# Kernel tuning notes

Measured on AMD Instinct MI355X. Metric: run time of the kernel, lower is better.

The kernel has to match this reference:

```python
import jax, jax.numpy as jnp
import numpy as np
from jax import lax

P_COARSE, P_FINE = 8, 4
EMBED_DIM = 128


def _patchify(x, p):
    # torch unfold(kernel=p, stride=p) then transpose: [B, Hp*Wp, C*p*p]
    B, C, H, W = x.shape
    Hp, Wp = H // p, W // p
    t = x.reshape(B, C, Hp, p, Wp, p).transpose(0, 2, 4, 1, 3, 5)
    return t.reshape(B, Hp * Wp, C * p * p), Hp, Wp


def _edge_map(x):
    gray = x.mean(axis=1, keepdims=True)
    kx = jnp.array([[-1., 0., 1.], [-2., 0., 2.], [-1., 0., 1.]], gray.dtype)[None, None]
    ky = jnp.array([[-1., -2., -1.], [0., 0., 0.], [1., 2., 1.]], gray.dtype)[None, None]
    pad = [(1, 1), (1, 1)]
    sx = lax.conv_general_dilated(gray, kx, (1, 1), pad)
    sy = lax.conv_general_dilated(gray, ky, (1, 1), pad)
    e = jnp.sqrt(sx * sx + sy * sy)
    B, _, H, W = e.shape
    # avg_pool2d(4, stride=4)
    return e.reshape(B, 1, H // 4, 4, W // 4, 4).mean(axis=(3, 5))


def _compact(tok, m):
    # stream-compact masked rows to the front, zero-pad the rest (pad_sequence semantics, padded to full Nf)
    Nf, D = tok.shape
    pos = jnp.cumsum(m) - 1
    pos = jnp.where(m, pos, Nf)  # unmasked rows go to overflow slot
    out = jnp.zeros((Nf + 1, D), tok.dtype).at[pos].set(tok)
    return out[:Nf]


def setup_inputs() -> dict:
    key = jax.random.key(0)
    ks = jax.random.split(key, 6)
    D = EMBED_DIM
    pd_c = 1 * P_COARSE * P_COARSE
    pd_f = 1 * P_FINE * P_FINE
    return {
        "x": jax.random.normal(ks[0], (8, 1, 512, 512), jnp.float32),
        "w_coarse": jax.random.normal(ks[1], (pd_c, D), jnp.float32) / np.sqrt(pd_c),
        "b_coarse": jnp.zeros((D,), jnp.float32),
        "w_fine": jax.random.normal(ks[2], (pd_f, D), jnp.float32) / np.sqrt(pd_f),
        "b_fine": jnp.zeros((D,), jnp.float32),
        "type_emb": jax.random.normal(ks[3], (2, D), jnp.float32) * 0.02,
    }


def reference(x, w_coarse, b_coarse, w_fine, b_fine, type_emb):
    B = x.shape[0]
    # coarse branch
    pc, Hc, Wc = _patchify(x, P_COARSE)
    coarse = pc @ w_coarse + b_coarse + type_emb[0]  # [B, Nc, D]
    # edge-driven mask
    edges = _edge_map(x)  # [B,1,He,We]
    mask = edges > edges.mean(axis=(2, 3), keepdims=True)
    # fine branch
    pf, Hf, Wf = _patchify(x, P_FINE)
    fine = pf @ w_fine + b_fine  # [B, Nf, D]
    # nearest upsample mask to (Hf, Wf): integer factor repeat
    m = mask[:, 0]
    m = jnp.repeat(jnp.repeat(m, Hf // m.shape[1], axis=1), Wf // m.shape[2], axis=2)
    mask_flat = m.reshape(B, -1)  # [B, Nf]
    fine_c = jax.vmap(_compact)(fine, mask_flat) + type_emb[1]
    tokens = jnp.concatenate([coarse, fine_c], axis=1)
    return tokens, mask_flat
```

## Files before the change

### kernel.cpp

```cpp
#include <hip/hip_runtime.h>

#define IMH 512
#define IMW 512
#define BATCH 8
#define NTOK 20480
#define NC 4096
#define NF 16384
#define ED 128

typedef float vf4 __attribute__((ext_vector_type(4)));

__device__ __forceinline__ void nt_store4v(float* p, float4 v) {
    vf4 t = {v.x, v.y, v.z, v.w};
    __builtin_nontemporal_store(t, (vf4*)p);
}

__global__ __launch_bounds__(256) void k1_edge_coarse(const float* __restrict__ x,
                                                      const float* __restrict__ wc,
                                                      const float* __restrict__ bc,
                                                      const float* __restrict__ temb,
                                                      float* __restrict__ out,
                                                      double* __restrict__ edges,
                                                      double* __restrict__ tsum) {
    __shared__ float esm[66][68];
    __shared__ double dred[4];
    int blk = blockIdx.x;
    int t = threadIdx.x;
    int lane = t & 63, wid = t >> 6;
    if (blk < 1024) {
        int b = blk >> 7;
        int pblk = (blk & 127) * 32;
        int wv = __builtin_amdgcn_readfirstlane(t >> 6);
        int h = wv & 1;
        int p0 = pblk + (wv >> 1) * 16;
        int d = h * 64 + lane;
        float wcol[64];
        #pragma unroll
        for (int k = 0; k < 64; ++k) wcol[k] = wc[k * ED + d];
        float base = bc[d] + temb[d];
        const float* img = x + ((size_t)b * IMH + (p0 >> 6) * 8) * IMW + (p0 & 63) * 8;
        float* dst = out + ((size_t)b * NTOK + p0) * ED + d;
        #pragma unroll
        for (int p = 0; p < 16; ++p) {
            const float* pimg = img + p * 8;
            float acc = base;
            #pragma unroll
            for (int r = 0; r < 8; ++r) {
                const float* rp = pimg + r * IMW;
                acc += rp[0] * wcol[r * 8 + 0] + rp[1] * wcol[r * 8 + 1]
                     + rp[2] * wcol[r * 8 + 2] + rp[3] * wcol[r * 8 + 3]
                     + rp[4] * wcol[r * 8 + 4] + rp[5] * wcol[r * 8 + 5]
                     + rp[6] * wcol[r * 8 + 6] + rp[7] * wcol[r * 8 + 7];
            }
            __builtin_nontemporal_store(acc, dst + (size_t)p * ED);
        }
    } else {
        int blk2 = blk - 1024;
        int b = blk2 >> 6;
        int tile = blk2 & 63;
        int ty0 = (tile >> 3) * 64;
        int tx0 = (tile & 7) * 64;
        const float* img = x + (size_t)b * (IMH * IMW);
        for (int idx = t; idx < 66 * 66; idx += 256) {
            int r = idx / 66, c = idx - r * 66;
            int gy = ty0 - 1 + r, gx = tx0 - 1 + c;
            float v = 0.f;
            if (gy >= 0 && gy < IMH && gx >= 0 && gx < IMW) v = img[gy * IMW + gx];
            esm[r][c] = v;
        }
        __syncthreads();
        int cy = t >> 4, cx = t & 15;
        double acc = 0.0;
        #pragma unroll
        for (int dy = 0; dy < 4; ++dy) {
            int py = cy * 4 + dy + 1;
            #pragma unroll
            for (int dx = 0; dx < 4; ++dx) {
                int px = cx * 4 + dx + 1;
                double a00 = (double)esm[py - 1][px - 1];
                double a01 = (double)esm[py - 1][px];
                double a02 = (double)esm[py - 1][px + 1];
                double a10 = (double)esm[py][px - 1];
                double a12 = (double)esm[py][px + 1];
                double a20 = (double)esm[py + 1][px - 1];
                double a21 = (double)esm[py + 1][px];
                double a22 = (double)esm[py + 1][px + 1];
                double sx = (a02 + 2.0 * a12 + a22) - (a00 + 2.0 * a10 + a20);
                double sy = (a20 + 2.0 * a21 + a22) - (a00 + 2.0 * a01 + a02);
                acc += sqrt(sx * sx + sy * sy);
            }
        }
        double cell = acc * (1.0 / 16.0);
        int gy = (ty0 >> 2) + cy;
        int gx = (tx0 >> 2) + cx;
        edges[((size_t)b << 14) + gy * 128 + gx] = cell;
        double sc = cell;
        #pragma unroll
        for (int off = 32; off > 0; off >>= 1) sc += __shfl_xor(sc, off);
        if (lane == 0) dred[wid] = sc;
        __syncthreads();
        if (t == 0) tsum[b * 64 + tile] = dred[0] + dred[1] + dred[2] + dred[3];
    }
}

__global__ __launch_bounds__(256) void k_scan(const double* __restrict__ edges,
                                              const double* __restrict__ tsum,
                                              unsigned long long* __restrict__ halfbits,
                                              int* __restrict__ halfbase,
                                              int* __restrict__ Kout,
                                              float* __restrict__ mask_out) {
    int b = blockIdx.x;
    int t = threadIdx.x;
    int lane = t & 63, wid = t >> 6;
    __shared__ unsigned long long hb_s[256];
    __shared__ int wtot[4];

    const double* ts = tsum + b * 64;
    double total = 0.0;
    #pragma unroll
    for (int j = 0; j < 64; ++j) total += ts[j];
    double mean = total * (1.0 / 16384.0);

    const double* e = edges + ((size_t)b << 14);
    float* mb = mask_out + ((size_t)b << 14);
    #pragma unroll 8
    for (int j = 0; j < 64; ++j) {
        double v = e[j * 256 + t];
        bool sel = v > mean;
        unsigned long long bal = __ballot(sel);
        if (lane == 0) hb_s[j * 4 + wid] = bal;
        __builtin_nontemporal_store(sel ? 1.0f : 0.0f, mb + j * 256 + t);
    }
    __syncthreads();
    unsigned long long myb = hb_s[t];
    int cnt = __popcll(myb);
    int incl = cnt;
    #pragma unroll
    for (int off = 1; off < 64; off <<= 1) {
        int up = __shfl_up(incl, off);
        if (lane >= off) incl += up;
    }
    if (lane == 63) wtot[wid] = incl;
    __syncthreads();
    int woff = 0;
    #pragma unroll
    for (int w = 0; w < 4; ++w) { if (w < wid) woff += wtot[w]; }
    int excl = woff + incl - cnt;
    halfbits[b * 256 + t] = myb;
    halfbase[b * 256 + t] = excl;
    if (t == 255) Kout[b] = excl + cnt;
}

__global__ __launch_bounds__(256) void k_fine(const float* __restrict__ x,
                                              const float* __restrict__ wfp,
                                              const float* __restrict__ bfp,
                                              const float* __restrict__ temb,
                                              const unsigned long long* __restrict__ halfbits,
                                              const int* __restrict__ halfbase,
                                              const int* __restrict__ Kout,
                                              float* __restrict__ out) {
    int b = blockIdx.y;
    int bx = blockIdx.x;
    int t = threadIdx.x;
    __shared__ float smx[4][256];

    unsigned long long bits = halfbits[b * 256 + bx];
    int base = halfbase[b * 256 + bx];
    int K = Kout[b];

    int irow = (bx >> 1) * 4;
    int icol = (bx & 1) * 256;
    const float* img = x + ((size_t)b * IMH + irow) * IMW + icol;
    {
        int r = t >> 6, c4 = t & 63;
        *(float4*)&smx[r][c4 * 4] = *(const float4*)&img[r * IMW + c4 * 4];
    }
    __syncthreads();

    int d4 = t & 31;
    int g = t >> 5;
    float4 wcol[16];
    #pragma unroll
    for (int k = 0; k < 16; ++k) wcol[k] = *(const float4*)&wfp[k * ED + d4 * 4];
    float4 fill = *(const float4*)&temb[ED + d4 * 4];
    float4 bse = *(const float4*)&bfp[d4 * 4];
    float4 fbase = make_float4(bse.x + fill.x, bse.y + fill.y, bse.z + fill.z, bse.w + fill.w);
    float* tok = out + ((size_t)b * NTOK + NC) * ED;
    int i0 = bx * 64;
    #pragma unroll
    for (int pp = 0; pp < 8; ++pp) {
        int p = g + pp * 8;
        int i = i0 + p;
        if ((bits >> p) & 1ULL) {
            int below = __popcll(bits & ((1ULL << p) - 1ULL));
            int ps = base + below;
            float4 acc = fbase;
            #pragma unroll
            for (int r = 0; r < 4; ++r) {
                float4 vv = *(const float4*)&smx[r][p * 4];
                acc.x += vv.x * wcol[4 * r].x + vv.y * wcol[4 * r + 1].x + vv.z * wcol[4 * r + 2].x + vv.w * wcol[4 * r + 3].x;
                acc.y += vv.x * wcol[4 * r].y + vv.y * wcol[4 * r + 1].y + vv.z * wcol[4 * r + 2].y + vv.w * wcol[4 * r + 3].y;
                acc.z += vv.x * wcol[4 * r].z + vv.y * wcol[4 * r + 1].z + vv.z * wcol[4 * r + 2].z + vv.w * wcol[4 * r + 3].z;
                acc.w += vv.x * wcol[4 * r].w + vv.y * wcol[4 * r + 1].w + vv.z * wcol[4 * r + 2].w + vv.w * wcol[4 * r + 3].w;
            }
            nt_store4v(tok + ((size_t)ps * 32 + d4) * 4, acc);
        }
        if (i >= K) {
            nt_store4v(tok + ((size_t)i * 32 + d4) * 4, fill);
        }
    }
}

extern "C" void kernel_launch(void* const* d_in, const int* in_sizes, int n_in,
                              void* d_out, int out_size, void* d_ws, size_t ws_size,
                              hipStream_t stream) {
    const float* x    = (const float*)d_in[0];
    const float* wc   = (const float*)d_in[1];
    const float* bc   = (const float*)d_in[2];
    const float* wfp  = (const float*)d_in[3];
    const float* bfp  = (const float*)d_in[4];
    const float* temb = (const float*)d_in[5];
    float* out = (float*)d_out;

    char* wsb = (char*)d_ws;
    double* edges = (double*)wsb;
    double* tsum  = (double*)(wsb + (size_t)BATCH * NF * 8);
    unsigned long long* halfbits = (unsigned long long*)(wsb + (size_t)BATCH * NF * 8 + 4096);
    int* halfbase = (int*)(wsb + (size_t)BATCH * NF * 8 + 4096 + 16384);
    int* Kout     = (int*)(wsb + (size_t)BATCH * NF * 8 + 4096 + 16384 + 8192);
    float* mask_out = out + (size_t)BATCH * NTOK * ED;

    k1_edge_coarse<<<dim3(1536), 256, 0, stream>>>(x, wc, bc, temb, out, edges, tsum);
    k_scan<<<dim3(BATCH), 256, 0, stream>>>(edges, tsum, halfbits, halfbase, Kout, mask_out);
    k_fine<<<dim3(256, BATCH), 256, 0, stream>>>(x, wfp, bfp, temb, halfbits, halfbase, Kout, out);
}
```

Before: 58.76 us.

## Fuse scan into edge kernel via last-block atomic counter; drop nontemporal stores

Merges the per-batch threshold/scan kernel into the edge/coarse kernel: each edge tile block increments a per-batch counter, and the last block to finish runs the mask and prefix-scan work. This removes one kernel launch and its serialization gap, at the cost of a memset launch and fences. It also replaces the nontemporal stores with ordinary stores for the coarse tokens, the mask and the fine tokens, which changes cache behaviour for the large output writes.

Result: slower. 88.34 us (+50.4%).

```diff
diff --git a/kernel.cpp b/kernel.cpp
--- a/kernel.cpp
+++ b/kernel.cpp
@@ -8,22 +8,23 @@
 #define NF 16384
 #define ED 128
 
-typedef float vf4 __attribute__((ext_vector_type(4)));
-
-__device__ __forceinline__ void nt_store4v(float* p, float4 v) {
-    vf4 t = {v.x, v.y, v.z, v.w};
-    __builtin_nontemporal_store(t, (vf4*)p);
-}
-
-__global__ __launch_bounds__(256) void k1_edge_coarse(const float* __restrict__ x,
-                                                      const float* __restrict__ wc,
-                                                      const float* __restrict__ bc,
-                                                      const float* __restrict__ temb,
-                                                      float* __restrict__ out,
-                                                      double* __restrict__ edges,
-                                                      double* __restrict__ tsum) {
+__global__ __launch_bounds__(256) void k1_all(const float* __restrict__ x,
+                                              const float* __restrict__ wc,
+                                              const float* __restrict__ bc,
+                                              const float* __restrict__ temb,
+                                              float* __restrict__ out,
+                                              double* __restrict__ edges,
+                                              double* __restrict__ tsum,
+                                              unsigned long long* __restrict__ halfbits,
+                                              int* __restrict__ halfbase,
+                                              int* __restrict__ Kout,
+                                              int* __restrict__ done,
+                                              float* __restrict__ mask_out) {
     __shared__ float esm[66][68];
     __shared__ double dred[4];
+    __shared__ unsigned long long hb_s[256];
+    __shared__ int wtot[4];
+    __shared__ int flag_s;
     int blk = blockIdx.x;
     int t = threadIdx.x;
     int lane = t & 63, wid = t >> 6;
@@ -52,14 +53,16 @@
                      + rp[4] * wcol[r * 8 + 4] + rp[5] * wcol[r * 8 + 5]
                      + rp[6] * wcol[r * 8 + 6] + rp[7] * wcol[r * 8 + 7];
             }
-            __builtin_nontemporal_store(acc, dst + (size_t)p * ED);
-        }
-    } else {
-        int blk2 = blk - 1024;
-        int b = blk2 >> 6;
-        int tile = blk2 & 63;
-        int ty0 = (tile >> 3) * 64;
-        int tx0 = (tile & 7) * 64;
+            dst[(size_t)p * ED] = acc;
+        }
+        return;
+    }
+    int blk2 = blk - 1024;
+    int b = blk2 >> 6;
+    int tile = blk2 & 63;
+    int ty0 = (tile >> 3) * 64;
+    int tx0 = (tile & 7) * 64;
+    {
         const float* img = x + (size_t)b * (IMH * IMW);
         for (int idx = t; idx < 66 * 66; idx += 256) {
             int r = idx / 66, c = idx - r * 66;
@@ -68,7 +71,9 @@
             if (gy >= 0 && gy < IMH && gx >= 0 && gx < IMW) v = img[gy * IMW + gx];
             esm[r][c] = v;
         }
-        __syncthreads();
+    }
+    __syncthreads();
+    {
         int cy = t >> 4, cx = t & 15;
         double acc = 0.0;
         #pragma unroll
@@ -98,29 +103,22 @@
         #pragma unroll
         for (int off = 32; off > 0; off >>= 1) sc += __shfl_xor(sc, off);
         if (lane == 0) dred[wid] = sc;
-        __syncthreads();
-        if (t == 0) tsum[b * 64 + tile] = dred[0] + dred[1] + dred[2] + dred[3];
-    }
-}
-
-__global__ __launch_bounds__(256) void k_scan(const double* __restrict__ edges,
-                                              const double* __restrict__ tsum,
-                                              unsigned long long* __restrict__ halfbits,
-                                              int* __restrict__ halfbase,
-                                              int* __restrict__ Kout,
-                                              float* __restrict__ mask_out) {
-    int b = blockIdx.x;
-    int t = threadIdx.x;
-    int lane = t & 63, wid = t >> 6;
-    __shared__ unsigned long long hb_s[256];
-    __shared__ int wtot[4];
-
+    }
+    __syncthreads();
+    if (t == 0) {
+        tsum[b * 64 + tile] = dred[0] + dred[1] + dred[2] + dred[3];
+        __threadfence();
+        int old = atomicAdd(done + b, 1);
+        flag_s = (old == 63) ? 1 : 0;
+    }
+    __syncthreads();
+    if (flag_s == 0) return;
+    __threadfence();
     const double* ts = tsum + b * 64;
     double total = 0.0;
     #pragma unroll
     for (int j = 0; j < 64; ++j) total += ts[j];
     double mean = total * (1.0 / 16384.0);
-
     const double* e = edges + ((size_t)b << 14);
     float* mb = mask_out + ((size_t)b << 14);
     #pragma unroll 8
@@ -129,7 +127,7 @@
         bool sel = v > mean;
         unsigned long long bal = __ballot(sel);
         if (lane == 0) hb_s[j * 4 + wid] = bal;
-        __builtin_nontemporal_store(sel ? 1.0f : 0.0f, mb + j * 256 + t);
+        mb[j * 256 + t] = sel ? 1.0f : 0.0f;
     }
     __syncthreads();
     unsigned long long myb = hb_s[t];
@@ -203,10 +201,10 @@
                 acc.z += vv.x * wcol[4 * r].z + vv.y * wcol[4 * r + 1].z + vv.z * wcol[4 * r + 2].z + vv.w * wcol[4 * r + 3].z;
                 acc.w += vv.x * wcol[4 * r].w + vv.y * wcol[4 * r + 1].w + vv.z * wcol[4 * r + 2].w + vv.w * wcol[4 * r + 3].w;
             }
-            nt_store4v(tok + ((size_t)ps * 32 + d4) * 4, acc);
+            *(float4*)(tok + ((size_t)ps * 32 + d4) * 4) = acc;
         }
         if (i >= K) {
-            nt_store4v(tok + ((size_t)i * 32 + d4) * 4, fill);
+            *(float4*)(tok + ((size_t)i * 32 + d4) * 4) = fill;
         }
     }
 }
@@ -223,14 +221,18 @@
     float* out = (float*)d_out;
 
     char* wsb = (char*)d_ws;
-    double* edges = (double*)wsb;
-    double* tsum  = (double*)(wsb + (size_t)BATCH * NF * 8);
-    unsigned long long* halfbits = (unsigned long long*)(wsb + (size_t)BATCH * NF * 8 + 4096);
-    int* halfbase = (int*)(wsb + (size_t)BATCH * NF * 8 + 4096 + 16384);
-    int* Kout     = (int*)(wsb + (size_t)BATCH * NF * 8 + 4096 + 16384 + 8192);
+    size_t off = 0;
+    double* edges = (double*)(wsb + off);            off += (size_t)BATCH * NF * 8;
+    double* tsum  = (double*)(wsb + off);            off += 4096;
+    unsigned long long* halfbits = (unsigned long long*)(wsb + off); off += (size_t)BATCH * 256 * 8;
+    int* halfbase = (int*)(wsb + off);               off += (size_t)BATCH * 256 * 4;
+    int* Kout     = (int*)(wsb + off);               off += 64;
+    int* done     = (int*)(wsb + off);               off += 64;
     float* mask_out = out + (size_t)BATCH * NTOK * ED;
 
-    k1_edge_coarse<<<dim3(1536), 256, 0, stream>>>(x, wc, bc, temb, out, edges, tsum);
-    k_scan<<<dim3(BATCH), 256, 0, stream>>>(edges, tsum, halfbits, halfbase, Kout, mask_out);
-    k_fine<<<dim3(256, BATCH), 256, 0, stream>>>(x, wfp, bfp, temb, halfbits, halfbase, Kout, out);
+    hipMemsetAsync(done, 0, BATCH * sizeof(int), stream);
+    k1_all<<<dim3(1536), 256, 0, stream>>>(x, wc, bc, temb, out, edges, tsum,
+                                           halfbits, halfbase, Kout, done, mask_out);
+    k_fine<<<dim3(256, BATCH), 256, 0, stream>>>(x, wfp, bfp, temb,
+                                                 halfbits, halfbase, Kout, out);
 }
```
